# Performance work log

Hardware: AMD Instinct MI355X
Metric: run time of the kernel (lower is better)

## Reference

```python
import jax, jax.numpy as jnp
import numpy as np

# Model dims (from ModelArgs defaults)
B, S, DIM = 1, 1024, 2880
H, HKV, HD = 64, 8, 64        # query heads, kv heads, head dim
GROUP = H // HKV              # 8 query heads per kv head
WINDOW = 128                  # sliding window (layer_idx=0 -> active)
THETA = 150000.0


def setup_inputs() -> dict:
    key = jax.random.key(0)
    ks = jax.random.split(key, 10)
    rn = lambda k, shape, sc: (jax.random.normal(k, shape, jnp.float32) * sc)
    return {
        "x": rn(ks[0], (B, S, DIM), 1.0),
        "wq_w": rn(ks[1], (H * HD, DIM), 0.02),
        "wq_b": rn(ks[2], (H * HD,), 0.02),
        "wk_w": rn(ks[3], (HKV * HD, DIM), 0.02),
        "wk_b": rn(ks[4], (HKV * HD,), 0.02),
        "wv_w": rn(ks[5], (HKV * HD, DIM), 0.02),
        "wv_b": rn(ks[6], (HKV * HD,), 0.02),
        "wo_w": rn(ks[7], (DIM, H * HD), 0.02),
        "wo_b": rn(ks[8], (DIM,), 0.02),
        "sinks": rn(ks[9], (H,), 1.0),
    }


def _rope(t):
    # t: [B, S, h, HD]; half-split (rotate_half) RoPE with base THETA
    half = HD // 2
    inv_freq = 1.0 / (THETA ** (jnp.arange(half, dtype=jnp.float32) * 2.0 / HD))
    ang = jnp.arange(S, dtype=jnp.float32)[:, None] * inv_freq      # [S, half]
    cos = jnp.cos(ang)[None, :, None, :]
    sin = jnp.sin(ang)[None, :, None, :]
    t1, t2 = t[..., :half], t[..., half:]
    return jnp.concatenate([t1 * cos - t2 * sin, t1 * sin + t2 * cos], axis=-1)


def reference(x, wq_w, wq_b, wk_w, wk_b, wv_w, wv_b, wo_w, wo_b, sinks):
    # Projections (nn.Linear: y = x @ W^T + b)
    q = (jnp.einsum('bsd,ed->bse', x, wq_w) + wq_b).reshape(B, S, H, HD)
    k = (jnp.einsum('bsd,ed->bse', x, wk_w) + wk_b).reshape(B, S, HKV, HD)
    v = (jnp.einsum('bsd,ed->bse', x, wv_w) + wv_b).reshape(B, S, HKV, HD)

    q = _rope(q)
    k = _rope(k)

    # GQA: expand kv heads to match query heads
    k = jnp.repeat(k, GROUP, axis=2)   # [B, S, H, HD]
    v = jnp.repeat(v, GROUP, axis=2)

    scale = HD ** -0.5
    scores = jnp.einsum('bihd,bjhd->bhij', q, k) * scale   # [B, H, S, S]

    # Causal + sliding-window mask: attend to j with 0 <= i-j < WINDOW
    i = jnp.arange(S)[:, None]
    j = jnp.arange(S)[None, :]
    allowed = (j <= i) & ((i - j) < WINDOW)
    scores = jnp.where(allowed, scores, jnp.float32(-1e30))

    # Softmax with per-head learnable sink logit folded into normalization
    sink = sinks[None, :, None, None]                       # [1, H, 1, 1]
    m = jnp.maximum(jnp.max(scores, axis=-1, keepdims=True), sink)
    e = jnp.exp(scores - m)
    denom = jnp.sum(e, axis=-1, keepdims=True) + jnp.exp(sink - m)
    probs = e / denom                                       # sink mass dropped

    out = jnp.einsum('bhij,bjhd->bihd', probs, v).reshape(B, S, H * HD)
    return jnp.einsum('bse,de->bsd', out, wo_w) + wo_b
```

## Files before the change

### kernel.cpp

```cpp
#include <hip/hip_runtime.h>

typedef __attribute__((ext_vector_type(4))) float f32x4;
typedef __attribute__((ext_vector_type(8))) short s16x8;
typedef unsigned short u16;

#define DEVI __device__ __forceinline__

DEVI u16 f2bf(float f) {
    union { float f; unsigned int u; } v; v.f = f;
    unsigned int r = v.u + 0x7FFFu + ((v.u >> 16) & 1u);
    return (u16)(r >> 16);
}
DEVI float bf2f(u16 b) {
    union { unsigned int u; float f; } v; v.u = ((unsigned int)b) << 16;
    return v.f;
}

typedef __attribute__((address_space(1))) void gv_t;
typedef __attribute__((address_space(3))) void sv_t;

#define GLOAD16(SRC, DST) __builtin_amdgcn_global_load_lds( \
    (gv_t*)(SRC), (sv_t*)(DST), 16, 0, 0)

DEVI f32x4 mfma_bf16(s16x8 a, s16x8 b, f32x4 c) {
    return __builtin_amdgcn_mfma_f32_16x16x32_bf16(a, b, c, 0, 0, 0);
}

__global__ void cvt_all_kernel(
    const float* __restrict__ x,  const float* __restrict__ wq, const float* __restrict__ wk,
    const float* __restrict__ wv, const float* __restrict__ wo,
    u16* __restrict__ xb, u16* __restrict__ wqb, u16* __restrict__ wkb,
    u16* __restrict__ wvb, u16* __restrict__ wob)
{
    int id = blockIdx.x * 256 + threadIdx.x;
    const float* s; u16* d; int off;
    if      (id < 737280)  { s = x;  d = xb;  off = id; }
    else if (id < 3686400) { s = wq; d = wqb; off = id - 737280; }
    else if (id < 4055040) { s = wk; d = wkb; off = id - 3686400; }
    else if (id < 4423680) { s = wv; d = wvb; off = id - 4055040; }
    else                   { s = wo; d = wob; off = id - 4423680; }
    f32x4 v = *(const f32x4*)(s + (size_t)off * 4);
    union { u16 u[4]; unsigned long long ll; } o;
    #pragma unroll
    for (int j = 0; j < 4; ++j) o.u[j] = f2bf(v[j]);
    *(unsigned long long*)(d + (size_t)off * 4) = o.ll;
}

__global__ __launch_bounds__(256, 3) void gemm_m97(
    const u16* __restrict__ A, int lda, int kit, int ntot,
    const u16* __restrict__ W0, int t0, int n0, int c0,
    const u16* __restrict__ W1, int t1, int n1, int c1,
    const u16* __restrict__ W2, int t2, int n2, int c2,
    u16* __restrict__ C, int ldc, long long cstride)
{
    __shared__ u16 Als[128 * 64];
    __shared__ u16 Bls[128 * 64];

    const int lin = blockIdx.x;
    const int xc  = lin & 7;
    const int mm  = lin >> 3;
    const int nbl = xc + 8 * (mm >> 3);
    const int yt  = mm & 7;
    if (nbl >= ntot) return;

    const int tid  = threadIdx.x;
    const int lane = tid & 63;
    const int wid  = tid >> 6;
    const int li   = lane & 15;
    const int lg   = lane >> 4;
    const int m0   = yt * 128;

    const u16* W; int nt0, nsz, cb;
    if (nbl < t0)           { W = W0; nt0 = nbl * 128;             nsz = n0; cb = c0; }
    else if (nbl < t0 + t1) { W = W1; nt0 = (nbl - t0) * 128;      nsz = n1; cb = c1; }
    else                    { W = W2; nt0 = (nbl - t0 - t1) * 128; nsz = n2; cb = c2; }

    const int z  = blockIdx.z;
    const int S  = gridDim.z;
    const int it0 = (z * kit) / S;
    const int it1 = ((z + 1) * kit) / S;
    u16* Cp = C + (long long)z * cstride;

    const int wm = (wid >> 1) * 64;
    const int wn = (wid & 1) * 64;

    f32x4 acc[4][4];
    #pragma unroll
    for (int mi = 0; mi < 4; ++mi)
        #pragma unroll
        for (int ni = 0; ni < 4; ++ni)
            acc[mi][ni] = (f32x4){0.f, 0.f, 0.f, 0.f};

    const int srow = tid >> 3;
    const int slc  = (tid & 7) ^ (srow & 7);

    for (int it = it0; it < it1; ++it) {
        const int k0 = it * 64;
        #pragma unroll
        for (int s_ = 0; s_ < 4; ++s_) {
            const u16* sa = A + (size_t)(m0 + s_ * 32 + srow) * lda + k0 + slc * 8;
            GLOAD16(sa, &Als[(s_ * 256 + tid) * 8]);
        }
        #pragma unroll
        for (int s_ = 0; s_ < 4; ++s_) {
            int wr = nt0 + s_ * 32 + srow;
            if (wr > nsz - 1) wr = nsz - 1;
            const u16* sb = W + (size_t)wr * lda + k0 + slc * 8;
            GLOAD16(sb, &Bls[(s_ * 256 + tid) * 8]);
        }
        __syncthreads();

        s16x8 af[4][2], bfv[4][2];
        #pragma unroll
        for (int mi = 0; mi < 4; ++mi)
            #pragma unroll
            for (int kc = 0; kc < 2; ++kc) {
                int row = wm + mi * 16 + li;
                int ch  = (kc * 4 + lg) ^ (row & 7);
                af[mi][kc] = *(const s16x8*)&Als[row * 64 + ch * 8];
            }
        #pragma unroll
        for (int ni = 0; ni < 4; ++ni)
            #pragma unroll
            for (int kc = 0; kc < 2; ++kc) {
                int row = wn + ni * 16 + li;
                int ch  = (kc * 4 + lg) ^ (row & 7);
                bfv[ni][kc] = *(const s16x8*)&Bls[row * 64 + ch * 8];
            }
        #pragma unroll
        for (int mi = 0; mi < 4; ++mi)
            #pragma unroll
            for (int ni = 0; ni < 4; ++ni)
                #pragma unroll
                for (int kc = 0; kc < 2; ++kc)
                    acc[mi][ni] = mfma_bf16(af[mi][kc], bfv[ni][kc], acc[mi][ni]);
        __syncthreads();
    }

    #pragma unroll
    for (int ni = 0; ni < 4; ++ni) {
        int colr = nt0 + wn + ni * 16 + li;
        if (colr < nsz) {
            #pragma unroll
            for (int mi = 0; mi < 4; ++mi)
                #pragma unroll
                for (int r = 0; r < 4; ++r) {
                    int row = m0 + wm + mi * 16 + lg * 4 + r;
                    Cp[(size_t)row * ldc + cb + colr] = f2bf(acc[mi][ni][r]);
                }
        }
    }
}

__global__ void rope_kernel(const u16* __restrict__ qkvp,
                            const float* __restrict__ qb, const float* __restrict__ kb,
                            const float* __restrict__ vb,
                            u16* __restrict__ qo, u16* __restrict__ ko, u16* __restrict__ vo)
{
    const long long PST = 1024LL * 5120;
    int id = blockIdx.x * 256 + threadIdx.x;
    int s  = id / 352;
    int g  = id % 352;
    const u16* r0 = qkvp + (size_t)s * 5120;

    if (g < 288) {
        bool isq = g < 256;
        int gg   = isq ? g : g - 256;
        int hh   = gg >> 2;
        int dg   = gg & 3;
        int col0 = (isq ? 0 : 4096) + hh * 64 + dg * 8;
        int bcol = isq ? col0 : col0 - 4096;
        const float* bias = isq ? qb : kb;

        float t1[8], t2[8];
        #pragma unroll
        for (int e = 0; e < 8; ++e) { t1[e] = bias[bcol + e]; t2[e] = bias[bcol + 32 + e]; }
        #pragma unroll
        for (int p = 0; p < 3; ++p) {
            s16x8 lo = *(const s16x8*)(r0 + col0 + p * PST);
            s16x8 hi = *(const s16x8*)(r0 + col0 + 32 + p * PST);
            #pragma unroll
            for (int e = 0; e < 8; ++e) {
                t1[e] += bf2f((u16)lo[e]);
                t2[e] += bf2f((u16)hi[e]);
            }
        }
        float sc = isq ? 0.125f : 1.0f;
        s16x8 o1, o2;
        #pragma unroll
        for (int e = 0; e < 8; ++e) {
            int d = dg * 8 + e;
            float ang = (float)s * exp2f((float)d * -0.5373314f);
            float sn, cs;
            sincosf(ang, &sn, &cs);
            o1[e] = (short)f2bf((t1[e] * cs - t2[e] * sn) * sc);
            o2[e] = (short)f2bf((t1[e] * sn + t2[e] * cs) * sc);
        }
        u16* dst = isq ? qo : ko;
        int ldd  = isq ? 4096 : 512;
        *(s16x8*)(dst + (size_t)s * ldd + bcol)      = o1;
        *(s16x8*)(dst + (size_t)s * ldd + bcol + 32) = o2;
    } else {
        int gg   = g - 288;
        int col0 = 4608 + gg * 8;
        float t[8];
        #pragma unroll
        for (int e = 0; e < 8; ++e) t[e] = vb[gg * 8 + e];
        #pragma unroll
        for (int p = 0; p < 3; ++p) {
            s16x8 v = *(const s16x8*)(r0 + col0 + p * PST);
            #pragma unroll
            for (int e = 0; e < 8; ++e) t[e] += bf2f((u16)v[e]);
        }
        s16x8 o;
        #pragma unroll
        for (int e = 0; e < 8; ++e) o[e] = (short)f2bf(t[e]);
        *(s16x8*)(vo + (size_t)s * 512 + gg * 8) = o;
    }
}

__global__ void reduce_out_kernel(const u16* __restrict__ parts,
                                  const float* __restrict__ bias,
                                  float* __restrict__ out)
{
    int id = blockIdx.x * 256 + threadIdx.x;
    const long long stride = 1024LL * 2880;
    long long base = (long long)id * 8;
    float s[8];
    #pragma unroll
    for (int j = 0; j < 8; ++j) s[j] = 0.f;
    #pragma unroll
    for (int p = 0; p < 5; ++p) {
        s16x8 v = *(const s16x8*)(parts + p * stride + base);
        #pragma unroll
        for (int j = 0; j < 8; ++j) s[j] += bf2f((u16)v[j]);
    }
    int cb = (int)(base % 2880);
    f32x4 b0 = *(const f32x4*)(bias + cb);
    f32x4 b1 = *(const f32x4*)(bias + cb + 4);
    f32x4 o0 = {s[0] + b0[0], s[1] + b0[1], s[2] + b0[2], s[3] + b0[3]};
    f32x4 o1 = {s[4] + b1[0], s[5] + b1[1], s[6] + b1[2], s[7] + b1[3]};
    *(f32x4*)(out + base)     = o0;
    *(f32x4*)(out + base + 4) = o1;
}

__global__ __launch_bounds__(256, 2) void attn_kernel(
    const u16* __restrict__ Q, const u16* __restrict__ Kb, const u16* __restrict__ Vb,
    const float* __restrict__ sinks, u16* __restrict__ Ob)
{
    __shared__ u16 Kls[64 * 64];
    __shared__ u16 Pls[4][16 * 72];

    const int h    = blockIdx.x;
    const int qblk = blockIdx.y;
    const int kvh  = h >> 3;
    const int tid  = threadIdx.x;
    const int lane = tid & 63;
    const int w    = tid >> 6;
    const int li   = lane & 15;
    const int lg   = lane >> 4;
    const int qw   = qblk * 64 + w * 16;

    s16x8 aq[2];
    {
        const u16* qrow = Q + ((size_t)(qw + li) * 64 + h) * 64 + lg * 8;
        aq[0] = *(const s16x8*)(qrow);
        aq[1] = *(const s16x8*)(qrow + 32);
    }

    const float snk = sinks[h];
    float m_run[4], l_run[4];
    f32x4 oacc[4];
    #pragma unroll
    for (int r = 0; r < 4; ++r) { m_run[r] = snk; l_run[r] = 1.0f; }
    #pragma unroll
    for (int ni = 0; ni < 4; ++ni) oacc[ni] = (f32x4){0.f, 0.f, 0.f, 0.f};

    const int srow = tid >> 3;
    const int slc  = (tid & 7) ^ (srow & 7);

    for (int t = 0; t < 3; ++t) {
        int jt = qblk - 2 + t;
        if (jt < 0) continue;
        int j0 = jt * 64;

        #pragma unroll
        for (int it = 0; it < 2; ++it) {
            const u16* src = Kb + ((size_t)(j0 + it * 32 + srow) * 8 + kvh) * 64 + slc * 8;
            GLOAD16(src, &Kls[(it * 256 + w * 64) * 8]);
        }
        __syncthreads();

        f32x4 sc[4];
        #pragma unroll
        for (int nf = 0; nf < 4; ++nf) {
            sc[nf] = (f32x4){0.f, 0.f, 0.f, 0.f};
            #pragma unroll
            for (int kc = 0; kc < 2; ++kc) {
                int row = nf * 16 + li;
                int ch  = (kc * 4 + lg) ^ (row & 7);
                s16x8 bk = *(const s16x8*)&Kls[row * 64 + ch * 8];
                sc[nf] = mfma_bf16(aq[kc], bk, sc[nf]);
            }
        }

        #pragma unroll
        for (int r = 0; r < 4; ++r) {
            const int qg = qw + lg * 4 + r;
            float mx = -1e30f;
            #pragma unroll
            for (int nf = 0; nf < 4; ++nf) {
                int jg = j0 + nf * 16 + li;
                bool ok = (jg <= qg) && (qg - jg < 128);
                float v = ok ? sc[nf][r] : -1e30f;
                sc[nf][r] = v;
                mx = fmaxf(mx, v);
            }
            #pragma unroll
            for (int off = 1; off < 16; off <<= 1)
                mx = fmaxf(mx, __shfl_xor(mx, off));
            float mnew = fmaxf(m_run[r], mx);
            float corr = __expf(m_run[r] - mnew);
            m_run[r] = mnew;
            float rs = 0.f;
            #pragma unroll
            for (int nf = 0; nf < 4; ++nf) {
                float p = __expf(sc[nf][r] - mnew);
                rs += p;
                Pls[w][(lg * 4 + r) * 72 + nf * 16 + li] = f2bf(p);
            }
            #pragma unroll
            for (int off = 1; off < 16; off <<= 1)
                rs += __shfl_xor(rs, off);
            l_run[r] = l_run[r] * corr + rs;
            #pragma unroll
            for (int ni = 0; ni < 4; ++ni) oacc[ni][r] *= corr;
        }
        __syncthreads();

        #pragma unroll
        for (int kc = 0; kc < 2; ++kc) {
            s16x8 pa = *(const s16x8*)&Pls[w][li * 72 + kc * 32 + lg * 8];
            #pragma unroll
            for (int ni = 0; ni < 4; ++ni) {
                const u16* vsrc = Vb + ((size_t)(j0 + kc * 32 + lg * 8) * 8 + kvh) * 64 + ni * 16 + li;
                s16x8 bv;
                #pragma unroll
                for (int i = 0; i < 8; ++i) bv[i] = (short)vsrc[(size_t)i * 512];
                oacc[ni] = mfma_bf16(pa, bv, oacc[ni]);
            }
        }
    }

    #pragma unroll
    for (int r = 0; r < 4; ++r) {
        float inv = 1.0f / l_run[r];
        #pragma unroll
        for (int ni = 0; ni < 4; ++ni)
            Ob[((size_t)(qw + lg * 4 + r) * 64 + h) * 64 + ni * 16 + li] = f2bf(oacc[ni][r] * inv);
    }
}

extern "C" void kernel_launch(void* const* d_in, const int* in_sizes, int n_in,
                              void* d_out, int out_size, void* d_ws, size_t ws_size,
                              hipStream_t stream)
{
    const float* x     = (const float*)d_in[0];
    const float* wq_w  = (const float*)d_in[1];
    const float* wq_b  = (const float*)d_in[2];
    const float* wk_w  = (const float*)d_in[3];
    const float* wk_b  = (const float*)d_in[4];
    const float* wv_w  = (const float*)d_in[5];
    const float* wv_b  = (const float*)d_in[6];
    const float* wo_w  = (const float*)d_in[7];
    const float* wo_b  = (const float*)d_in[8];
    const float* sinks = (const float*)d_in[9];

    char* ws = (char*)d_ws;
    u16*   xb   = (u16*)(ws + 0);
    u16*   wqb  = (u16*)(ws + 5898240ULL);
    u16*   wkb  = (u16*)(ws + 29491200ULL);
    u16*   wvb  = (u16*)(ws + 32440320ULL);
    u16*   qkvp = (u16*)(ws + 35389440ULL);
    u16*   qr   = (u16*)(ws + 0);
    u16*   kr   = (u16*)(ws + 8388608ULL);
    u16*   vbf  = (u16*)(ws + 9437184ULL);
    u16*   attb = (u16*)(ws + 10485760ULL);
    u16*   oprt = (u16*)(ws + 58982400ULL);
    u16*   wob  = (u16*)(ws + 88473600ULL);

    (void)in_sizes; (void)n_in; (void)out_size; (void)ws_size;

    cvt_all_kernel<<<28800, 256, 0, stream>>>(x, wq_w, wk_w, wv_w, wo_w,
                                              xb, wqb, wkb, wvb, wob);
    gemm_m97<<<dim3(320, 1, 3), 256, 0, stream>>>(xb, 2880, 45, 40,
        wqb, 32, 4096, 0,
        wkb, 4, 512, 4096,
        wvb, 4, 512, 4608,
        qkvp, 5120, 1024LL * 5120);
    rope_kernel<<<1408, 256, 0, stream>>>(qkvp, wq_b, wk_b, wv_b, qr, kr, vbf);
    attn_kernel<<<dim3(64, 16), 256, 0, stream>>>(qr, kr, vbf, sinks, attb);
    gemm_m97<<<dim3(192, 1, 5), 256, 0, stream>>>(attb, 4096, 64, 23,
        wob, 23, 2880, 0,
        wob, 0, 0, 0,
        wob, 0, 0, 0,
        oprt, 2880, 1024LL * 2880);
    reduce_out_kernel<<<1440, 256, 0, stream>>>(oprt, wo_b, (float*)d_out);
}
```

Baseline: 130.9 us.

## Overlap wo weight conversion with QKV GEMM via extra conversion blocks

Moves the fp32-to-bf16 conversion of the output-projection weight out of the upfront conversion kernel and into extra blocks appended to the QKV GEMM grid. Only the z=0 slice of those extra blocks does conversion work; the rest exit immediately. The aim is to shrink the serial conversion kernel and hide the wo conversion behind the memory-light parts of the GEMM. In exchange, the extra blocks compete with GEMM blocks for bandwidth and CU slots, and idle blocks add launch overhead.

```diff
diff --git a/kernel.cpp b/kernel.cpp
--- a/kernel.cpp
+++ b/kernel.cpp
@@ -26,19 +26,18 @@
     return __builtin_amdgcn_mfma_f32_16x16x32_bf16(a, b, c, 0, 0, 0);
 }
 
-__global__ void cvt_all_kernel(
+__global__ void cvt1_kernel(
     const float* __restrict__ x,  const float* __restrict__ wq, const float* __restrict__ wk,
-    const float* __restrict__ wv, const float* __restrict__ wo,
+    const float* __restrict__ wv,
     u16* __restrict__ xb, u16* __restrict__ wqb, u16* __restrict__ wkb,
-    u16* __restrict__ wvb, u16* __restrict__ wob)
+    u16* __restrict__ wvb)
 {
     int id = blockIdx.x * 256 + threadIdx.x;
     const float* s; u16* d; int off;
     if      (id < 737280)  { s = x;  d = xb;  off = id; }
     else if (id < 3686400) { s = wq; d = wqb; off = id - 737280; }
     else if (id < 4055040) { s = wk; d = wkb; off = id - 3686400; }
-    else if (id < 4423680) { s = wv; d = wvb; off = id - 4055040; }
-    else                   { s = wo; d = wob; off = id - 4423680; }
+    else                   { s = wv; d = wvb; off = id - 4055040; }
     f32x4 v = *(const f32x4*)(s + (size_t)off * 4);
     union { u16 u[4]; unsigned long long ll; } o;
     #pragma unroll
@@ -47,16 +46,37 @@
 }
 
 __global__ __launch_bounds__(256, 3) void gemm_m97(
-    const u16* __restrict__ A, int lda, int kit, int ntot,
+    const u16* __restrict__ A, int lda, int kit, int ntot, int gemmx,
     const u16* __restrict__ W0, int t0, int n0, int c0,
     const u16* __restrict__ W1, int t1, int n1, int c1,
     const u16* __restrict__ W2, int t2, int n2, int c2,
-    u16* __restrict__ C, int ldc, long long cstride)
+    u16* __restrict__ C, int ldc, long long cstride,
+    const float* __restrict__ cvsrc, u16* __restrict__ cvdst, int cvblk)
 {
     __shared__ u16 Als[128 * 64];
     __shared__ u16 Bls[128 * 64];
 
     const int lin = blockIdx.x;
+    const int z   = blockIdx.z;
+
+    if (lin >= gemmx) {
+        if (z == 0 && cvblk > 0) {
+            const int cb_  = lin - gemmx;
+            const int step = cvblk * 256;
+            int idx = cb_ * 256 + threadIdx.x;
+            #pragma unroll 4
+            for (int i = 0; i < 16; ++i) {
+                f32x4 v = *(const f32x4*)(cvsrc + (size_t)idx * 4);
+                union { u16 u[4]; unsigned long long ll; } o;
+                #pragma unroll
+                for (int j = 0; j < 4; ++j) o.u[j] = f2bf(v[j]);
+                *(unsigned long long*)(cvdst + (size_t)idx * 4) = o.ll;
+                idx += step;
+            }
+        }
+        return;
+    }
+
     const int xc  = lin & 7;
     const int mm  = lin >> 3;
     const int nbl = xc + 8 * (mm >> 3);
@@ -75,7 +95,6 @@
     else if (nbl < t0 + t1) { W = W1; nt0 = (nbl - t0) * 128;      nsz = n1; cb = c1; }
     else                    { W = W2; nt0 = (nbl - t0 - t1) * 128; nsz = n2; cb = c2; }
 
-    const int z  = blockIdx.z;
     const int S  = gridDim.z;
     const int it0 = (z * kit) / S;
     const int it1 = ((z + 1) * kit) / S;
@@ -391,19 +410,20 @@
 
     (void)in_sizes; (void)n_in; (void)out_size; (void)ws_size;
 
-    cvt_all_kernel<<<28800, 256, 0, stream>>>(x, wq_w, wk_w, wv_w, wo_w,
-                                              xb, wqb, wkb, wvb, wob);
-    gemm_m97<<<dim3(320, 1, 3), 256, 0, stream>>>(xb, 2880, 45, 40,
+    cvt1_kernel<<<17280, 256, 0, stream>>>(x, wq_w, wk_w, wv_w, xb, wqb, wkb, wvb);
+    gemm_m97<<<dim3(1040, 1, 3), 256, 0, stream>>>(xb, 2880, 45, 40, 320,
         wqb, 32, 4096, 0,
         wkb, 4, 512, 4096,
         wvb, 4, 512, 4608,
-        qkvp, 5120, 1024LL * 5120);
+        qkvp, 5120, 1024LL * 5120,
+        wo_w, wob, 720);
     rope_kernel<<<1408, 256, 0, stream>>>(qkvp, wq_b, wk_b, wv_b, qr, kr, vbf);
     attn_kernel<<<dim3(64, 16), 256, 0, stream>>>(qr, kr, vbf, sinks, attb);
-    gemm_m97<<<dim3(192, 1, 5), 256, 0, stream>>>(attb, 4096, 64, 23,
+    gemm_m97<<<dim3(192, 1, 5), 256, 0, stream>>>(attb, 4096, 64, 23, 192,
         wob, 23, 2880, 0,
         wob, 0, 0, 0,
         wob, 0, 0, 0,
-        oprt, 2880, 1024LL * 2880);
+        oprt, 2880, 1024LL * 2880,
+        (const float*)nullptr, (u16*)nullptr, 0);
     reduce_out_kernel<<<1440, 256, 0, stream>>>(oprt, wo_b, (float*)d_out);
 }
```

Measured after the change: 130.3 us. About the same (-0.5%).
